# Kernel tuning notes

Hardware: AMD Instinct MI355X
Metric: run time of the kernel (lower is better)

The kernel has to match this reference:

```python
import jax, jax.numpy as jnp
import numpy as np

B, C_IN, N, K, S, C_OUT = 256, 8, 4096, 9, 2, 8

def setup_inputs() -> dict:
    key = jax.random.key(0)
    k1, k2, k3, k4, k5 = jax.random.split(key, 5)
    scale = (1.0 / (C_IN * K)) ** 0.5  # matches uniform(-sqrt(k), sqrt(k)) magnitude
    x = jax.random.normal(k1, (B, C_IN, N), dtype=jnp.float32)
    neighborhoods = jax.random.randint(k2, (N, K), 0, N, dtype=jnp.int32)
    sub_ids = jax.random.randint(k3, (N,), 0, S, dtype=jnp.int32)
    weight = jax.random.uniform(k4, (S, C_IN, K, C_OUT), dtype=jnp.float32, minval=-scale, maxval=scale)
    bias = jax.random.uniform(k5, (S, C_OUT), dtype=jnp.float32, minval=-scale, maxval=scale)
    return {"x": x, "neighborhoods": neighborhoods, "sub_ids": sub_ids, "weight": weight, "bias": bias}

def reference(x, neighborhoods, sub_ids, weight, bias):
    # x: [B, C_in, N]; neighborhoods: [N, K]; sub_ids: [N]
    # weight: [S, C_in, K, C_out]; bias: [S, C_out]
    rel = x[:, :, neighborhoods]            # [B, C_in, N, K]  (per-site neighbor gather)
    w_site = weight[sub_ids]                # [N, C_in, K, C_out] (per-site sublattice weight)
    out = jnp.einsum('bcnk,nckd->bdn', rel, w_site)  # [B, C_out, N]
    out = out + bias[sub_ids].T[None]       # broadcast [1, C_out, N]
    return out
```

## Files before the change

kernel.cpp:

```cpp
#include <hip/hip_runtime.h>
#include <stdint.h>
#include <stddef.h>

#define BSZ  256
#define NSZ  4096
#define CIN  8
#define KNB  9
#define DOUT 8
#define NSUB 2

typedef __fp16   fh2  __attribute__((ext_vector_type(2)));
typedef __fp16   v8fh __attribute__((ext_vector_type(8)));
typedef float    f4   __attribute__((ext_vector_type(4)));
typedef uint32_t u32x4 __attribute__((ext_vector_type(4)));

#define BTAB_U32 (NSUB * 3 * 64 * 4)
#define BOFF     ((NSZ + 1) * 4)

static __device__ __forceinline__ uint32_t pk_f16(float a, float b) {
    fh2 h = __builtin_amdgcn_cvt_pkrtz(a, b);
    return __builtin_bit_cast(uint32_t, h);
}

__global__ __launch_bounds__(1024) void latconv_kernel(
    const float* __restrict__ x, const int* __restrict__ nbh,
    const int* __restrict__ sub, const float* __restrict__ w,
    const float* __restrict__ bias, float* __restrict__ out)
{
    __shared__ __align__(16) uint32_t xl[BOFF + BTAB_U32];

    const int b    = blockIdx.x & 255;
    const int half = blockIdx.x >> 8;
    const int t    = threadIdx.x;
    const float* xb = x + (size_t)b * (CIN * NSZ);

    if (t < NSUB * 3 * 64) {
        const int lane2 = t & 63, s = (t >> 6) % 3, sg = t / 192;
        const int g2 = lane2 >> 4, d2 = lane2 & 15, ks = s * 4 + g2;
        u32x4 row;
        #pragma unroll
        for (int cp = 0; cp < 4; ++cp) {
            float v0 = 0.f, v1 = 0.f;
            if (d2 < DOUT && ks < KNB) {
                v0 = w[((sg * CIN + 2 * cp    ) * KNB + ks) * DOUT + d2];
                v1 = w[((sg * CIN + 2 * cp + 1) * KNB + ks) * DOUT + d2];
            }
            row[cp] = pk_f16(v0, v1);
        }
        *reinterpret_cast<u32x4*>(&xl[BOFF + 4 * (size_t)t]) = row;
    }

    {
        const int j0 = 4 * t;
        f4 v[CIN];
        #pragma unroll
        for (int c = 0; c < CIN; ++c)
            v[c] = *reinterpret_cast<const f4*>(xb + c * NSZ + j0);
        #pragma unroll
        for (int jj = 0; jj < 4; ++jj) {
            u32x4 row;
            #pragma unroll
            for (int cp = 0; cp < 4; ++cp)
                row[cp] = pk_f16(v[2 * cp][jj], v[2 * cp + 1][jj]);
            *reinterpret_cast<u32x4*>(&xl[(size_t)(j0 + jj) * 4]) = row;
        }
    }
    if (t == 0) {
        u32x4 z = { 0, 0, 0, 0 };
        *reinterpret_cast<u32x4*>(&xl[(size_t)NSZ * 4]) = z;
    }

    const int lane = t & 63, wv = t >> 6;
    const int g = lane >> 4, r = lane & 15, d = r;

    const float bz0 = bias[d & 7];
    const float bz1 = bias[DOUT + (d & 7)];

    __syncthreads();

    u32x4 bf[2][3];
    #pragma unroll
    for (int sg = 0; sg < 2; ++sg)
        #pragma unroll
        for (int s = 0; s < 3; ++s)
            bf[sg][s] = *reinterpret_cast<const u32x4*>(
                &xl[BOFF + 4 * (size_t)((sg * 3 + s) * 64 + lane)]);

    const char* xlb = reinterpret_cast<const char*>(xl);
    #pragma unroll 2
    for (int tile = 0; tile < 8; ++tile) {
        const int n0 = half * 2048 + wv * 128 + tile * 16;

        const int4 sv = *reinterpret_cast<const int4*>(sub + n0 + g * 4);

        int js[3];
        #pragma unroll
        for (int s = 0; s < 3; ++s) {
            const int ks = s * 4 + g;
            js[s] = (ks < KNB) ? nbh[(n0 + r) * KNB + ks] : NSZ;
        }

        f4 a0 = { 0.f, 0.f, 0.f, 0.f };
        f4 a1 = { 0.f, 0.f, 0.f, 0.f };
        #pragma unroll
        for (int s = 0; s < 3; ++s) {
            const u32x4 av = *reinterpret_cast<const u32x4*>(xlb + ((size_t)(uint32_t)js[s] << 4));
            const v8fh af = __builtin_bit_cast(v8fh, av);
            a0 = __builtin_amdgcn_mfma_f32_16x16x32_f16(af, __builtin_bit_cast(v8fh, bf[0][s]), a0, 0, 0, 0);
            a1 = __builtin_amdgcn_mfma_f32_16x16x32_f16(af, __builtin_bit_cast(v8fh, bf[1][s]), a1, 0, 0, 0);
        }

        if (d < DOUT) {
            const int svv[4] = { sv.x, sv.y, sv.z, sv.w };
            f4 o;
            #pragma unroll
            for (int reg = 0; reg < 4; ++reg) {
                const float acc = svv[reg] ? a1[reg] : a0[reg];
                o[reg] = acc + (svv[reg] ? bz1 : bz0);
            }
            *reinterpret_cast<f4*>(out + ((size_t)b * DOUT + d) * NSZ + n0 + g * 4) = o;
        }
    }
}

extern "C" void kernel_launch(void* const* d_in, const int* in_sizes, int n_in,
                              void* d_out, int out_size, void* d_ws, size_t ws_size,
                              hipStream_t stream) {
    const float* x    = (const float*)d_in[0];
    const int*   nbh  = (const int*)d_in[1];
    const int*   sub  = (const int*)d_in[2];
    const float* w    = (const float*)d_in[3];
    const float* bias = (const float*)d_in[4];
    float* out = (float*)d_out;
    (void)d_ws; (void)ws_size;

    latconv_kernel<<<2 * BSZ, 1024, 0, stream>>>(x, nbh, sub, w, bias, out);
}
```

Measured before the change: 101.6 us.

## Process full site range per block and preload neighbor indices before barrier

Each block now covers all 4096 sites of one batch instead of half, so the LDS staging of x (converted to fp16) happens once per batch rather than twice. Neighbor indices and sublattice bits for all 16 tiles are loaded into registers before the barrier, overlapping those global loads with the staging. Sublattice ids are packed into bitmasks, and the launch bound asks for multiple waves per SIMD. The trade-offs are higher register pressure from the 48 preloaded indices, a grid of 256 blocks that may underfill the GPU's CUs, and longer serial work per block.

```diff
diff --git a/kernel.cpp b/kernel.cpp
--- a/kernel.cpp
+++ b/kernel.cpp
@@ -22,16 +22,15 @@
     return __builtin_bit_cast(uint32_t, h);
 }
 
-__global__ __launch_bounds__(1024) void latconv_kernel(
+__global__ __launch_bounds__(1024, 4) void latconv_kernel(
     const float* __restrict__ x, const int* __restrict__ nbh,
     const int* __restrict__ sub, const float* __restrict__ w,
     const float* __restrict__ bias, float* __restrict__ out)
 {
     __shared__ __align__(16) uint32_t xl[BOFF + BTAB_U32];
 
-    const int b    = blockIdx.x & 255;
-    const int half = blockIdx.x >> 8;
-    const int t    = threadIdx.x;
+    const int b = blockIdx.x;
+    const int t = threadIdx.x;
     const float* xb = x + (size_t)b * (CIN * NSZ);
 
     if (t < NSUB * 3 * 64) {
@@ -73,6 +72,24 @@
     const int lane = t & 63, wv = t >> 6;
     const int g = lane >> 4, r = lane & 15, d = r;
 
+    uint32_t js[16][3];
+    uint32_t smask_lo = 0, smask_hi = 0;
+    #pragma unroll
+    for (int tile = 0; tile < 16; ++tile) {
+        const int n0 = wv * 256 + tile * 16;
+        #pragma unroll
+        for (int s = 0; s < 3; ++s) {
+            const int ks = s * 4 + g;
+            const int j = (ks < KNB) ? nbh[(n0 + r) * KNB + ks] : NSZ;
+            js[tile][s] = (uint32_t)j << 4;
+        }
+        const int4 sv = *reinterpret_cast<const int4*>(sub + n0 + g * 4);
+        const uint32_t bits = (uint32_t)((sv.x & 1) | ((sv.y & 1) << 1) |
+                                         ((sv.z & 1) << 2) | ((sv.w & 1) << 3));
+        if (tile < 8) smask_lo |= bits << (4 * tile);
+        else          smask_hi |= bits << (4 * (tile - 8));
+    }
+
     const float bz0 = bias[d & 7];
     const float bz1 = bias[DOUT + (d & 7)];
 
@@ -87,36 +104,28 @@
                 &xl[BOFF + 4 * (size_t)((sg * 3 + s) * 64 + lane)]);
 
     const char* xlb = reinterpret_cast<const char*>(xl);
-    #pragma unroll 2
-    for (int tile = 0; tile < 8; ++tile) {
-        const int n0 = half * 2048 + wv * 128 + tile * 16;
-
-        const int4 sv = *reinterpret_cast<const int4*>(sub + n0 + g * 4);
-
-        int js[3];
-        #pragma unroll
-        for (int s = 0; s < 3; ++s) {
-            const int ks = s * 4 + g;
-            js[s] = (ks < KNB) ? nbh[(n0 + r) * KNB + ks] : NSZ;
-        }
+    #pragma unroll
+    for (int tile = 0; tile < 16; ++tile) {
+        const int n0 = wv * 256 + tile * 16;
 
         f4 a0 = { 0.f, 0.f, 0.f, 0.f };
         f4 a1 = { 0.f, 0.f, 0.f, 0.f };
         #pragma unroll
         for (int s = 0; s < 3; ++s) {
-            const u32x4 av = *reinterpret_cast<const u32x4*>(xlb + ((size_t)(uint32_t)js[s] << 4));
+            const u32x4 av = *reinterpret_cast<const u32x4*>(xlb + js[tile][s]);
             const v8fh af = __builtin_bit_cast(v8fh, av);
             a0 = __builtin_amdgcn_mfma_f32_16x16x32_f16(af, __builtin_bit_cast(v8fh, bf[0][s]), a0, 0, 0, 0);
             a1 = __builtin_amdgcn_mfma_f32_16x16x32_f16(af, __builtin_bit_cast(v8fh, bf[1][s]), a1, 0, 0, 0);
         }
 
         if (d < DOUT) {
-            const int svv[4] = { sv.x, sv.y, sv.z, sv.w };
+            const uint32_t bits = (tile < 8) ? (smask_lo >> (4 * tile))
+                                             : (smask_hi >> (4 * (tile - 8)));
             f4 o;
             #pragma unroll
             for (int reg = 0; reg < 4; ++reg) {
-                const float acc = svv[reg] ? a1[reg] : a0[reg];
-                o[reg] = acc + (svv[reg] ? bz1 : bz0);
+                const bool s1 = (bits >> reg) & 1;
+                o[reg] = (s1 ? a1[reg] : a0[reg]) + (s1 ? bz1 : bz0);
             }
             *reinterpret_cast<f4*>(out + ((size_t)b * DOUT + d) * NSZ + n0 + g * 4) = o;
         }
@@ -134,5 +143,5 @@
     float* out = (float*)d_out;
     (void)d_ws; (void)ws_size;
 
-    latconv_kernel<<<2 * BSZ, 1024, 0, stream>>>(x, nbh, sub, w, bias, out);
+    latconv_kernel<<<BSZ, 1024, 0, stream>>>(x, nbh, sub, w, bias, out);
 }
```

Result: slower. 109.6 us (+7.8%).
